# Optimization experiments

Hardware: AMD Instinct MI355X
Metric: run time of the kernel (lower is better)

The kernel has to match this reference:

```python
import jax, jax.numpy as jnp
import numpy as np
from jax.ops import segment_sum, segment_max

NUM_USERS = 100000
NUM_ITEMS = 50000
N_TOTAL = NUM_USERS + NUM_ITEMS
D = 64
E = 2000000
GCN_LAYERS = 3
GCN_LEFT = 0.5
GCN_RIGHT = 0.5
GCN_MEAN = True
USE_CL = True
CL_EPS = 0.2
CL_LAYER = 1
RF_LAYERS = 2
RF_TAU = 0.5
RF_ALPHA = 1.0


def setup_inputs() -> dict:
    key = jax.random.key(0)
    k1, k2, k3, k4, k5 = jax.random.split(key, 5)
    return {
        "user_emb": 0.1 * jax.random.normal(k1, (NUM_USERS, D), dtype=jnp.float32),
        "item_emb": 0.1 * jax.random.normal(k2, (NUM_ITEMS, D), dtype=jnp.float32),
        "noise": jax.random.uniform(k3, (GCN_LAYERS, N_TOTAL, D), dtype=jnp.float32),
        "edge_u": jax.random.randint(k4, (E,), 0, NUM_USERS, dtype=jnp.int32),
        "edge_i": jax.random.randint(k5, (E,), 0, NUM_ITEMS, dtype=jnp.int32),
    }


def _gcn_layer(emb, edge_u, edge_i, cu, ci):
    # LightGCN-style degree-normalized bipartite propagation over the edge list.
    ue, ie = emb[:NUM_USERS], emb[NUM_USERS:]
    # messages item -> user and user -> item, normalized by deg^-left * deg^-right
    msg_u = segment_sum(ie[edge_i] * (cu[edge_u] * ci[edge_i])[:, None], edge_u,
                        num_segments=NUM_USERS)
    msg_i = segment_sum(ue[edge_u] * (ci[edge_i] * cu[edge_u])[:, None], edge_i,
                        num_segments=NUM_ITEMS)
    return jnp.concatenate([msg_u, msg_i], axis=0)


def _rankformer_layer(emb, edge_u, edge_i):
    # Edge-sparse attention: per-edge score, segment softmax per node, weighted aggregate.
    ue, ie = emb[:NUM_USERS], emb[NUM_USERS:]
    eu_g, ei_g = ue[edge_u], ie[edge_i]            # [E, D] gathers
    s = RF_ALPHA * jnp.sum(eu_g * ei_g, axis=-1)   # [E]
    # user-side softmax over incident items
    mu = segment_max(s, edge_u, num_segments=NUM_USERS)
    pu = jnp.exp(s - mu[edge_u])
    zu = segment_sum(pu, edge_u, num_segments=NUM_USERS)
    rec_u = segment_sum(pu[:, None] * ei_g, edge_u, num_segments=NUM_USERS)
    rec_u = rec_u / jnp.maximum(zu, 1e-9)[:, None]
    # item-side softmax over incident users
    mi = segment_max(s, edge_i, num_segments=NUM_ITEMS)
    pi = jnp.exp(s - mi[edge_i])
    zi = segment_sum(pi, edge_i, num_segments=NUM_ITEMS)
    rec_i = segment_sum(pi[:, None] * eu_g, edge_i, num_segments=NUM_ITEMS)
    rec_i = rec_i / jnp.maximum(zi, 1e-9)[:, None]
    return jnp.concatenate([rec_u, rec_i], axis=0)


def reference(user_emb, item_emb, noise, edge_u, edge_i):
    ones = jnp.ones((E,), dtype=user_emb.dtype)
    du = jnp.maximum(segment_sum(ones, edge_u, num_segments=NUM_USERS), 1.0)
    di = jnp.maximum(segment_sum(ones, edge_i, num_segments=NUM_ITEMS), 1.0)
    cu = du ** (-GCN_LEFT)   # user-side normalization (left exponent)
    ci = di ** (-GCN_RIGHT)  # item-side normalization (right exponent)

    emb = jnp.concatenate([user_emb, item_emb], axis=0)  # [N_TOTAL, D]
    layer_embs = [emb]
    for layer in range(GCN_LAYERS):
        emb = _gcn_layer(emb, edge_u, edge_i, cu, ci)
        if USE_CL:
            nz = noise[layer]
            nz = nz / jnp.maximum(jnp.linalg.norm(nz, axis=-1, keepdims=True), 1e-12)
            emb = emb + jnp.sign(emb) * nz * CL_EPS
        layer_embs.append(emb)
    if GCN_MEAN:
        emb = jnp.mean(jnp.stack(layer_embs, axis=-1), axis=-1)

    for _ in range(RF_LAYERS):
        rec = _rankformer_layer(emb, edge_u, edge_i)
        emb = (1.0 - RF_TAU) * emb + RF_TAU * rec
    return emb
```

## Files before the change

kernel.cpp:

```cpp
#include <hip/hip_runtime.h>
#include <math.h>

#pragma clang fp contract(off)
#pragma clang fp reassociate(off)

#define NU 100000
#define NI 50000
#define NT 150000
#define DD 64
#define NE 2000000
#define NTD (NT * DD)
#define NPART 8
#define PARTW_U (NU / NPART)
#define PARTW_I (NI / NPART)
#define NCHUNK 256
#define CHW ((NE + NCHUNK - 1) / NCHUNK)

typedef _Float16 half4 __attribute__((ext_vector_type(4)));

__global__ __launch_bounds__(256) void count_ui_k(const int* __restrict__ eu, const int* __restrict__ ei,
                                                  int* __restrict__ cnt) {
  int part = blockIdx.x & 7;
  int side = (blockIdx.x >> 3) & 1;
  int chunk = blockIdx.x >> 4;
  int e0 = chunk * CHW;
  int e1 = e0 + CHW; if (e1 > NE) e1 = NE;
  if (side == 0) {
    int lo = part * PARTW_U, hi = lo + PARTW_U;
    for (int e = e0 + threadIdx.x; e < e1; e += 256) {
      int u = eu[e];
      if (u >= lo && u < hi) atomicAdd(&cnt[u], 1);
    }
  } else {
    int lo = part * PARTW_I, hi = lo + PARTW_I;
    for (int e = e0 + threadIdx.x; e < e1; e += 256) {
      int it = ei[e];
      if (it >= lo && it < hi) atomicAdd(&cnt[NU + it], 1);
    }
  }
}

__global__ __launch_bounds__(1024) void scanA_k(const int* __restrict__ cnt, int* __restrict__ lexcl,
                                                int* __restrict__ partials, int n) {
  int idx = blockIdx.x * 1024 + threadIdx.x;
  int v = (idx < n) ? cnt[idx] : 0;
  int lane = threadIdx.x & 63;
  int wid = threadIdx.x >> 6;
  int x = v;
#pragma unroll
  for (int off = 1; off < 64; off <<= 1) {
    int y = __shfl_up(x, off, 64);
    if (lane >= off) x += y;
  }
  __shared__ int wtot[16], woff[16];
  if (lane == 63) wtot[wid] = x;
  __syncthreads();
  if (threadIdx.x == 0) {
    int a = 0;
#pragma unroll
    for (int w = 0; w < 16; ++w) { woff[w] = a; a += wtot[w]; }
    partials[blockIdx.x] = a;
  }
  __syncthreads();
  if (idx < n) lexcl[idx] = x - v + woff[wid];
}

__global__ __launch_bounds__(64) void scanB_k(int* __restrict__ partials, int* __restrict__ row, int nchunks) {
  int lane = threadIdx.x;
  int carry = 0;
  for (int base = 0; base < nchunks; base += 64) {
    int idx = base + lane;
    int v = (idx < nchunks) ? partials[idx] : 0;
    int x = v;
#pragma unroll
    for (int off = 1; off < 64; off <<= 1) {
      int y = __shfl_up(x, off, 64);
      if (lane >= off) x += y;
    }
    if (idx < nchunks) partials[idx] = carry + x - v;
    carry += __shfl(x, 63, 64);
  }
  if (lane == 0) row[NT] = carry;
}

__global__ __launch_bounds__(1024) void scanC_k(int* __restrict__ row, int* __restrict__ cursor,
                                                float* __restrict__ coef, const int* __restrict__ partials, int n) {
  int idx = blockIdx.x * 1024 + threadIdx.x;
  if (idx >= n) return;
  int c = cursor[idx];
  int fin = row[idx] + partials[blockIdx.x];
  row[idx] = fin;
  cursor[idx] = fin;
  coef[idx] = (float)pow((double)(c > 0 ? c : 1), -0.5);
}

__global__ __launch_bounds__(256) void fill_ui_k(const int* __restrict__ eu, const int* __restrict__ ei,
                                                 int* __restrict__ cursor, int* __restrict__ eid) {
  int part = blockIdx.x & 7;
  int side = (blockIdx.x >> 3) & 1;
  int chunk = blockIdx.x >> 4;
  int e0 = chunk * CHW;
  int e1 = e0 + CHW; if (e1 > NE) e1 = NE;
  if (side == 0) {
    int lo = part * PARTW_U, hi = lo + PARTW_U;
    for (int e = e0 + threadIdx.x; e < e1; e += 256) {
      int u = eu[e];
      if (u >= lo && u < hi) {
        int p = atomicAdd(&cursor[u], 1);
        __builtin_nontemporal_store(e, &eid[p]);
      }
    }
  } else {
    int lo = part * PARTW_I, hi = lo + PARTW_I;
    for (int e = e0 + threadIdx.x; e < e1; e += 256) {
      int it = ei[e];
      if (it >= lo && it < hi) {
        int p = atomicAdd(&cursor[NU + it], 1);
        __builtin_nontemporal_store(e, &eid[p]);
      }
    }
  }
}

__global__ __launch_bounds__(256) void sort_k(const int* __restrict__ row, const int* __restrict__ eid,
                                              const int* __restrict__ eu, const int* __restrict__ ei,
                                              int* __restrict__ col) {
  int wv = (blockIdx.x * blockDim.x + threadIdx.x) >> 6;
  int lane = threadIdx.x & 63;
  if (wv >= NT) return;
  int beg = row[wv], end = row[wv + 1];
  for (int idx = beg + lane; idx < end; idx += 64) {
    int my = eid[idx];
    int r = 0;
    for (int j = beg; j < end; ++j) r += (eid[j] < my);
    col[beg + r] = (wv < NU) ? (NU + ei[my]) : eu[my];
  }
}

template <int FIRST, int LAST>
__global__ __launch_bounds__(256) void gcn4_k(const float* __restrict__ in, float* __restrict__ out,
                                              float* __restrict__ acc,
                                              const int* __restrict__ row, const int* __restrict__ col,
                                              const float* __restrict__ coef, const float* __restrict__ nz_l,
                                              const float* __restrict__ ue, const float* __restrict__ ie,
                                              _Float16* __restrict__ h16out) {
  int wave = (blockIdx.x * blockDim.x + threadIdx.x) >> 6;
  int lane = threadIdx.x & 63;
  int g = lane >> 4, q = lane & 15;
  int node = wave * 4 + g;
  if (node >= NT) return;
  int beg = row[node], end = row[node + 1];
  float cn = coef[node];
  float sx = 0.f, sy = 0.f, sz = 0.f, sw = 0.f;

  const float* gbase;
  if (FIRST) {
    gbase = (node < NU) ? (ie - (size_t)NU * DD) : ue;
  } else {
    gbase = in;
  }

#define GLD(dv, dc, kk) { int m_ = col[kk]; dc = coef[m_]; dv = *(const float4*)(gbase + (size_t)m_ * DD + q * 4); }
  float4 cv0, cv1, cv2, cv3;
  float cc0, cc1, cc2, cc3;
  int rem = end - beg;
  int k4end = end - (rem & 3);
  int k = beg;
  if (k < k4end) {
    GLD(cv0, cc0, k) GLD(cv1, cc1, k + 1) GLD(cv2, cc2, k + 2) GLD(cv3, cc3, k + 3)
  }
  for (; k < k4end; k += 4) {
    float4 nv0, nv1, nv2, nv3;
    float nc0, nc1, nc2, nc3;
    bool more = (k + 4) < k4end;
    if (more) {
      GLD(nv0, nc0, k + 4) GLD(nv1, nc1, k + 5) GLD(nv2, nc2, k + 6) GLD(nv3, nc3, k + 7)
    }
    {
      float w = cn * cc0;
      sx = sx + (cv0.x * w); sy = sy + (cv0.y * w); sz = sz + (cv0.z * w); sw = sw + (cv0.w * w);
    }
    {
      float w = cn * cc1;
      sx = sx + (cv1.x * w); sy = sy + (cv1.y * w); sz = sz + (cv1.z * w); sw = sw + (cv1.w * w);
    }
    {
      float w = cn * cc2;
      sx = sx + (cv2.x * w); sy = sy + (cv2.y * w); sz = sz + (cv2.z * w); sw = sw + (cv2.w * w);
    }
    {
      float w = cn * cc3;
      sx = sx + (cv3.x * w); sy = sy + (cv3.y * w); sz = sz + (cv3.z * w); sw = sw + (cv3.w * w);
    }
    if (more) {
      cv0 = nv0; cc0 = nc0; cv1 = nv1; cc1 = nc1;
      cv2 = nv2; cc2 = nc2; cv3 = nv3; cc3 = nc3;
    }
  }
  for (; k < end; ++k) {
    float4 v; float c;
    GLD(v, c, k)
    float w = cn * c;
    sx = sx + (v.x * w); sy = sy + (v.y * w); sz = sz + (v.z * w); sw = sw + (v.w * w);
  }
#undef GLD

  float4 nzv = *(const float4*)(nz_l + (size_t)node * DD + q * 4);
  float4 sq;
  sq.x = nzv.x * nzv.x; sq.y = nzv.y * nzv.y;
  sq.z = nzv.z * nzv.z; sq.w = nzv.w * nzv.w;
  float rA0 = 0.f, rA1 = 0.f, rA2 = 0.f, rA3 = 0.f;
  float rB0 = 0.f, rB1 = 0.f, rB2 = 0.f, rB3 = 0.f;
  int base = g * 16;
#pragma unroll
  for (int kk = 0; kk < 8; ++kk) {
    int le = base + 2 * kk, lo = le + 1;
    rA0 = rA0 + __shfl(sq.x, le, 64);
    rA1 = rA1 + __shfl(sq.y, le, 64);
    rA2 = rA2 + __shfl(sq.z, le, 64);
    rA3 = rA3 + __shfl(sq.w, le, 64);
    rB0 = rB0 + __shfl(sq.x, lo, 64);
    rB1 = rB1 + __shfl(sq.y, lo, 64);
    rB2 = rB2 + __shfl(sq.z, lo, 64);
    rB3 = rB3 + __shfl(sq.w, lo, 64);
  }
  float t01 = rA0 + rA1, t23 = rA2 + rA3;
  float t45 = rB0 + rB1, t67 = rB2 + rB3;
  float tot = (t01 + t23) + (t45 + t67);
  float nrm = __fsqrt_rn(tot);
  float den = fmaxf(nrm, 1e-12f);
  float4 o;
  {
    float nn = nzv.x / den;
    float sg = (sx > 0.f) ? 1.f : ((sx < 0.f) ? -1.f : 0.f);
    o.x = sx + ((sg * nn) * 0.2f);
  }
  {
    float nn = nzv.y / den;
    float sg = (sy > 0.f) ? 1.f : ((sy < 0.f) ? -1.f : 0.f);
    o.y = sy + ((sg * nn) * 0.2f);
  }
  {
    float nn = nzv.z / den;
    float sg = (sz > 0.f) ? 1.f : ((sz < 0.f) ? -1.f : 0.f);
    o.z = sz + ((sg * nn) * 0.2f);
  }
  {
    float nn = nzv.w / den;
    float sg = (sw > 0.f) ? 1.f : ((sw < 0.f) ? -1.f : 0.f);
    o.w = sw + ((sg * nn) * 0.2f);
  }
  size_t boff = (size_t)node * DD + q * 4;
  if (FIRST) {
    const float* ownp = (node < NU) ? (ue + (size_t)node * DD) : (ie + (size_t)(node - NU) * DD);
    float4 own = *(const float4*)(ownp + q * 4);
    *(float4*)(out + boff) = o;
    float4 a;
    a.x = own.x + o.x; a.y = own.y + o.y; a.z = own.z + o.z; a.w = own.w + o.w;
    *(float4*)(acc + boff) = a;
  } else {
    float4 a = *(const float4*)(acc + boff);
    if (LAST) {
      float4 mo;
      mo.x = (a.x + o.x) * 0.25f;
      mo.y = (a.y + o.y) * 0.25f;
      mo.z = (a.z + o.z) * 0.25f;
      mo.w = (a.w + o.w) * 0.25f;
      *(float4*)(out + boff) = mo;
      half4 hh;
      hh.x = (_Float16)mo.x; hh.y = (_Float16)mo.y;
      hh.z = (_Float16)mo.z; hh.w = (_Float16)mo.w;
      *(half4*)(h16out + boff) = hh;
    } else {
      *(float4*)(out + boff) = o;
      a.x = a.x + o.x; a.y = a.y + o.y; a.z = a.z + o.z; a.w = a.w + o.w;
      *(float4*)(acc + boff) = a;
    }
  }
}

template <int WRITEH>
__global__ __launch_bounds__(256) void rfaccum_k(const float* __restrict__ inF,
                                                 const _Float16* __restrict__ inH,
                                                 float* __restrict__ outF,
                                                 _Float16* __restrict__ outH,
                                                 const int* __restrict__ row, const int* __restrict__ col) {
  int wave = (blockIdx.x * blockDim.x + threadIdx.x) >> 6;
  int lane = threadIdx.x & 63;
  int g = lane >> 4, q = lane & 15;
  int node = wave * 4 + g;
  if (node >= NT) return;
  int beg = row[node], end = row[node + 1];
  size_t boff = (size_t)node * DD + q * 4;
  float4 e = *(const float4*)(inF + boff);
  float rx = 0.f, ry = 0.f, rz = 0.f, rw = 0.f, zacc = 0.f;

#define VLD(dv, kk) { dv = *(const half4*)(inH + (size_t)col[kk] * DD + q * 4); }
#define STEP(hv)                                                             \
  {                                                                          \
    float vx = (float)hv.x, vy = (float)hv.y, vz = (float)hv.z, vw = (float)hv.w; \
    float d = fmaf(e.x, vx, fmaf(e.y, vy, fmaf(e.z, vz, e.w * vw)));         \
    d += __shfl_xor(d, 1, 64); d += __shfl_xor(d, 2, 64);                    \
    d += __shfl_xor(d, 4, 64); d += __shfl_xor(d, 8, 64);                    \
    float p = __expf(d);                                                     \
    rx = fmaf(p, vx, rx); ry = fmaf(p, vy, ry);                              \
    rz = fmaf(p, vz, rz); rw = fmaf(p, vw, rw);                              \
    zacc = zacc + p;                                                         \
  }

  half4 cv0, cv1, cv2, cv3;
  int rem = end - beg;
  int k4end = end - (rem & 3);
  int k = beg;
  if (k < k4end) {
    VLD(cv0, k) VLD(cv1, k + 1) VLD(cv2, k + 2) VLD(cv3, k + 3)
  }
  for (; k < k4end; k += 4) {
    half4 nv0, nv1, nv2, nv3;
    bool more = (k + 4) < k4end;
    if (more) {
      VLD(nv0, k + 4) VLD(nv1, k + 5) VLD(nv2, k + 6) VLD(nv3, k + 7)
    }
    STEP(cv0) STEP(cv1) STEP(cv2) STEP(cv3)
    if (more) { cv0 = nv0; cv1 = nv1; cv2 = nv2; cv3 = nv3; }
  }
  for (; k < end; ++k) {
    half4 v;
    VLD(v, k)
    STEP(v)
  }
#undef STEP
#undef VLD

  float zi = 1.f / fmaxf(zacc, 1e-9f);
  float4 o;
  o.x = 0.5f * e.x + 0.5f * (rx * zi);
  o.y = 0.5f * e.y + 0.5f * (ry * zi);
  o.z = 0.5f * e.z + 0.5f * (rz * zi);
  o.w = 0.5f * e.w + 0.5f * (rw * zi);
  *(float4*)(outF + boff) = o;
  if (WRITEH) {
    half4 hh;
    hh.x = (_Float16)o.x; hh.y = (_Float16)o.y;
    hh.z = (_Float16)o.z; hh.w = (_Float16)o.w;
    *(half4*)(outH + boff) = hh;
  }
}

extern "C" void kernel_launch(void* const* d_in, const int* in_sizes, int n_in,
                              void* d_out, int out_size, void* d_ws, size_t ws_size,
                              hipStream_t stream) {
  const float* user_emb = (const float*)d_in[0];
  const float* item_emb = (const float*)d_in[1];
  const float* noise    = (const float*)d_in[2];
  const int*   edge_u   = (const int*)d_in[3];
  const int*   edge_i   = (const int*)d_in[4];
  float* out = (float*)d_out;

  float* embA = (float*)d_ws;
  float* embB = embA + (size_t)NTD;
  float* coef = embB + (size_t)NTD;
  int*   row  = (int*)(coef + (NT + 16));
  int*   cursor = row + (NT + 16);
  int*   partials = cursor + (NT + 16);
  int*   eidt = partials + 256;
  int*   col  = eidt + 2 * (size_t)NE;
  _Float16* H0 = (_Float16*)(col + 2 * (size_t)NE);
  _Float16* H1 = H0 + (size_t)NTD;

  float* acc = out;

  const int nchunks = (NT + 1023) / 1024;

  hipMemsetAsync(cursor, 0, (size_t)NT * sizeof(int), stream);
  count_ui_k<<<NCHUNK * NPART * 2, 256, 0, stream>>>(edge_u, edge_i, cursor);
  scanA_k<<<nchunks, 1024, 0, stream>>>(cursor, row, partials, NT);
  scanB_k<<<1, 64, 0, stream>>>(partials, row, nchunks);
  scanC_k<<<nchunks, 1024, 0, stream>>>(row, cursor, coef, partials, NT);
  fill_ui_k<<<NCHUNK * NPART * 2, 256, 0, stream>>>(edge_u, edge_i, cursor, eidt);

  const int gwave = (NT * 64 + 255) / 256;
  const int g4    = (NT / 4 * 64) / 256;

  sort_k<<<gwave, 256, 0, stream>>>(row, eidt, edge_u, edge_i, col);

  gcn4_k<1, 0><<<g4, 256, 0, stream>>>(nullptr, embB, acc, row, col, coef,
                                       noise + 0 * (size_t)NTD, user_emb, item_emb, nullptr);
  gcn4_k<0, 0><<<g4, 256, 0, stream>>>(embB, embA, acc, row, col, coef,
                                       noise + 1 * (size_t)NTD, user_emb, item_emb, nullptr);
  gcn4_k<0, 1><<<g4, 256, 0, stream>>>(embA, embB, acc, row, col, coef,
                                       noise + 2 * (size_t)NTD, user_emb, item_emb, H0);

  rfaccum_k<1><<<g4, 256, 0, stream>>>(embB, H0, embA, H1, row, col);
  rfaccum_k<0><<<g4, 256, 0, stream>>>(embA, H1, out, nullptr, row, col);
}
```

Measured before the change: 1.126 ms.

## Build CSR via two-level bucketed scatter instead of partitioned global atomics

Replaces the 8-way partitioned count and fill passes, which each reread the edge lists many times, with a coarse bucket pass. Edges are histogrammed into 200 node-range buckets in shared memory, prefix-scanned, and scattered as (node, edge) pairs. Per-bucket blocks then do the degree count and CSR placement with atomics on a localized node range. This cuts redundant edge reads and scatters global atomics, at the cost of extra kernels and a large temporary buffer that aliases the fp16 H buffers. BCAP has to cover the largest bucket.

```diff
diff --git a/kernel.cpp b/kernel.cpp
--- a/kernel.cpp
+++ b/kernel.cpp
@@ -10,33 +10,97 @@
 #define DD 64
 #define NE 2000000
 #define NTD (NT * DD)
-#define NPART 8
-#define PARTW_U (NU / NPART)
-#define PARTW_I (NI / NPART)
-#define NCHUNK 256
-#define CHW ((NE + NCHUNK - 1) / NCHUNK)
+
+#define NBUCK 200
+#define BW_U 1000
+#define BW_I 500
+#define BCAP 25600
+#define NBLK 1024
+#define CHW2 ((NE + NBLK - 1) / NBLK)
 
 typedef _Float16 half4 __attribute__((ext_vector_type(4)));
-
-__global__ __launch_bounds__(256) void count_ui_k(const int* __restrict__ eu, const int* __restrict__ ei,
-                                                  int* __restrict__ cnt) {
-  int part = blockIdx.x & 7;
-  int side = (blockIdx.x >> 3) & 1;
-  int chunk = blockIdx.x >> 4;
-  int e0 = chunk * CHW;
-  int e1 = e0 + CHW; if (e1 > NE) e1 = NE;
-  if (side == 0) {
-    int lo = part * PARTW_U, hi = lo + PARTW_U;
-    for (int e = e0 + threadIdx.x; e < e1; e += 256) {
-      int u = eu[e];
-      if (u >= lo && u < hi) atomicAdd(&cnt[u], 1);
-    }
-  } else {
-    int lo = part * PARTW_I, hi = lo + PARTW_I;
-    for (int e = e0 + threadIdx.x; e < e1; e += 256) {
-      int it = ei[e];
-      if (it >= lo && it < hi) atomicAdd(&cnt[NU + it], 1);
-    }
+typedef unsigned long long u64;
+
+__global__ __launch_bounds__(256) void histo_k(const int* __restrict__ eu, const int* __restrict__ ei,
+                                               int* __restrict__ hist) {
+  __shared__ int h[NBUCK];
+  for (int t = threadIdx.x; t < NBUCK; t += 256) h[t] = 0;
+  __syncthreads();
+  int e0 = blockIdx.x * CHW2;
+  int e1 = e0 + CHW2; if (e1 > NE) e1 = NE;
+  for (int e = e0 + threadIdx.x; e < e1; e += 256) {
+    atomicAdd(&h[eu[e] / BW_U], 1);
+    atomicAdd(&h[100 + ei[e] / BW_I], 1);
+  }
+  __syncthreads();
+  for (int t = threadIdx.x; t < NBUCK; t += 256) hist[blockIdx.x * NBUCK + t] = h[t];
+}
+
+__global__ __launch_bounds__(64) void hscan_k(int* __restrict__ hist, int* __restrict__ btot) {
+  int b = blockIdx.x;
+  int lane = threadIdx.x;
+  int vals[16];
+  int lsum = 0;
+#pragma unroll
+  for (int j = 0; j < 16; ++j) {
+    vals[j] = hist[(lane * 16 + j) * NBUCK + b];
+    lsum += vals[j];
+  }
+  int x = lsum;
+#pragma unroll
+  for (int off = 1; off < 64; off <<= 1) {
+    int y = __shfl_up(x, off, 64);
+    if (lane >= off) x += y;
+  }
+  int total = __shfl(x, 63, 64);
+  int run = b * BCAP + (x - lsum);
+#pragma unroll
+  for (int j = 0; j < 16; ++j) {
+    int v = vals[j];
+    hist[(lane * 16 + j) * NBUCK + b] = run;
+    run += v;
+  }
+  if (lane == 0) btot[b] = total;
+}
+
+__global__ __launch_bounds__(256) void scatter_k(const int* __restrict__ eu, const int* __restrict__ ei,
+                                                 const int* __restrict__ base, u64* __restrict__ bent) {
+  __shared__ int cur[NBUCK];
+  for (int t = threadIdx.x; t < NBUCK; t += 256) cur[t] = base[blockIdx.x * NBUCK + t];
+  __syncthreads();
+  int e0 = blockIdx.x * CHW2;
+  int e1 = e0 + CHW2; if (e1 > NE) e1 = NE;
+  for (int e = e0 + threadIdx.x; e < e1; e += 256) {
+    int u = eu[e];
+    int p0 = atomicAdd(&cur[u / BW_U], 1);
+    bent[p0] = ((u64)(unsigned)u << 32) | (unsigned)e;
+    int iv = ei[e];
+    int p1 = atomicAdd(&cur[100 + iv / BW_I], 1);
+    bent[p1] = ((u64)(unsigned)(NU + iv) << 32) | (unsigned)e;
+  }
+}
+
+__global__ __launch_bounds__(512) void bcount_k(const int* __restrict__ btot,
+                                                const u64* __restrict__ bent,
+                                                int* __restrict__ cnt) {
+  int b = blockIdx.x;
+  int n = btot[b];
+  const u64* src = bent + (size_t)b * BCAP;
+  for (int j = threadIdx.x; j < n; j += 512) {
+    atomicAdd(&cnt[(int)(src[j] >> 32)], 1);
+  }
+}
+
+__global__ __launch_bounds__(512) void place_k(const int* __restrict__ btot,
+                                               const u64* __restrict__ bent,
+                                               int* __restrict__ cursor, int* __restrict__ eid) {
+  int b = blockIdx.x;
+  int n = btot[b];
+  const u64* src = bent + (size_t)b * BCAP;
+  for (int j = threadIdx.x; j < n; j += 512) {
+    u64 v = src[j];
+    int p = atomicAdd(&cursor[(int)(v >> 32)], 1);
+    eid[p] = (int)(unsigned)v;
   }
 }
 
@@ -92,34 +156,6 @@
   row[idx] = fin;
   cursor[idx] = fin;
   coef[idx] = (float)pow((double)(c > 0 ? c : 1), -0.5);
-}
-
-__global__ __launch_bounds__(256) void fill_ui_k(const int* __restrict__ eu, const int* __restrict__ ei,
-                                                 int* __restrict__ cursor, int* __restrict__ eid) {
-  int part = blockIdx.x & 7;
-  int side = (blockIdx.x >> 3) & 1;
-  int chunk = blockIdx.x >> 4;
-  int e0 = chunk * CHW;
-  int e1 = e0 + CHW; if (e1 > NE) e1 = NE;
-  if (side == 0) {
-    int lo = part * PARTW_U, hi = lo + PARTW_U;
-    for (int e = e0 + threadIdx.x; e < e1; e += 256) {
-      int u = eu[e];
-      if (u >= lo && u < hi) {
-        int p = atomicAdd(&cursor[u], 1);
-        __builtin_nontemporal_store(e, &eid[p]);
-      }
-    }
-  } else {
-    int lo = part * PARTW_I, hi = lo + PARTW_I;
-    for (int e = e0 + threadIdx.x; e < e1; e += 256) {
-      int it = ei[e];
-      if (it >= lo && it < hi) {
-        int p = atomicAdd(&cursor[NU + it], 1);
-        __builtin_nontemporal_store(e, &eid[p]);
-      }
-    }
-  }
 }
 
 __global__ __launch_bounds__(256) void sort_k(const int* __restrict__ row, const int* __restrict__ eid,
@@ -363,9 +399,12 @@
   int*   row  = (int*)(coef + (NT + 16));
   int*   cursor = row + (NT + 16);
   int*   partials = cursor + (NT + 16);
-  int*   eidt = partials + 256;
+  int*   btot = partials + 256;
+  int*   hist = btot + 256;
+  int*   eidt = hist + NBLK * NBUCK;
   int*   col  = eidt + 2 * (size_t)NE;
-  _Float16* H0 = (_Float16*)(col + 2 * (size_t)NE);
+  u64*   bent = (u64*)(col + 2 * (size_t)NE);
+  _Float16* H0 = (_Float16*)bent;
   _Float16* H1 = H0 + (size_t)NTD;
 
   float* acc = out;
@@ -373,11 +412,15 @@
   const int nchunks = (NT + 1023) / 1024;
 
   hipMemsetAsync(cursor, 0, (size_t)NT * sizeof(int), stream);
-  count_ui_k<<<NCHUNK * NPART * 2, 256, 0, stream>>>(edge_u, edge_i, cursor);
+
+  histo_k<<<NBLK, 256, 0, stream>>>(edge_u, edge_i, hist);
+  hscan_k<<<NBUCK, 64, 0, stream>>>(hist, btot);
+  scatter_k<<<NBLK, 256, 0, stream>>>(edge_u, edge_i, hist, bent);
+  bcount_k<<<NBUCK, 512, 0, stream>>>(btot, bent, cursor);
   scanA_k<<<nchunks, 1024, 0, stream>>>(cursor, row, partials, NT);
   scanB_k<<<1, 64, 0, stream>>>(partials, row, nchunks);
   scanC_k<<<nchunks, 1024, 0, stream>>>(row, cursor, coef, partials, NT);
-  fill_ui_k<<<NCHUNK * NPART * 2, 256, 0, stream>>>(edge_u, edge_i, cursor, eidt);
+  place_k<<<NBUCK, 512, 0, stream>>>(btot, bent, cursor, eidt);
 
   const int gwave = (NT * 64 + 255) / 256;
   const int g4    = (NT / 4 * 64) / 256;
```

Measured after the change: 983.5 us. 12.6% less time.
